# Kernel tuning notes

Measured on AMD Instinct MI355X. Metric: run time of the kernel, lower is better.

The kernel has to match this reference:

```python
import jax, jax.numpy as jnp
import numpy as np

B, H, W, C = 4, 64, 64, 256
CK = C // 8  # f/g projection dim = 32


def setup_inputs() -> dict:
    key = jax.random.key(0)
    ks = jax.random.split(key, 4)
    x = jax.random.normal(ks[0], (B, H, W, C), dtype=jnp.float32)
    Wf = jax.random.normal(ks[1], (C, CK), dtype=jnp.float32) * (1.0 / np.sqrt(C))
    Wg = jax.random.normal(ks[2], (C, CK), dtype=jnp.float32) * (1.0 / np.sqrt(C))
    Wh = jax.random.normal(ks[3], (C, C), dtype=jnp.float32) * (1.0 / np.sqrt(C))
    bf = jnp.zeros((CK,), jnp.float32)
    bg = jnp.zeros((CK,), jnp.float32)
    bh = jnp.zeros((C,), jnp.float32)
    return {"x": x, "Wf": Wf, "bf": bf, "Wg": Wg, "bg": bg, "Wh": Wh, "bh": bh}


def reference(x, Wf, bf, Wg, bg, Wh, bh):
    b, h, w, c = x.shape
    n = h * w
    xf = x.reshape(b, n, c)  # 1x1 conv == per-pixel matmul
    f = xf @ Wf + bf         # [b, n, c/8]  (keys)
    g = xf @ Wg + bg         # [b, n, c/8]  (queries)
    hh = xf @ Wh + bh        # [b, n, c]    (values)
    # s[i,j] = g_i . f_j  (tf.matmul(g, f, transpose_b=True))
    s = jnp.einsum('bik,bjk->bij', g, f)
    beta = jax.nn.softmax(s, axis=-1)
    o = jnp.einsum('bij,bjc->bic', beta, hh)
    return x + o.reshape(b, h, w, c)
```

## Files before the change

kernel.cpp:

```cpp
#include <hip/hip_runtime.h>
#include <math.h>

#define CDIM 256
#define CKD  32
#define NPIX 4096
#define BATCH 4
#define NMACRO (NPIX / 64)

typedef __attribute__((ext_vector_type(8)))  short bf16x8;
typedef __attribute__((ext_vector_type(16))) float f32x16;

#if __has_builtin(__builtin_amdgcn_exp2f)
#define EXP2(x) __builtin_amdgcn_exp2f(x)
#else
#define EXP2(x) exp2f(x)
#endif

__device__ inline ushort f2bf(float x) {
    unsigned u = __float_as_uint(x);
    u += 0x7fffu + ((u >> 16) & 1u);
    return (ushort)(u >> 16);
}
__device__ inline unsigned packbf(float a, float b) {
    return (unsigned)f2bf(a) | ((unsigned)f2bf(b) << 16);
}
__device__ inline unsigned cvtpk(float a, float b) {
    unsigned r;
    asm("v_cvt_pk_bf16_f32 %0, %1, %2" : "=v"(r) : "v"(a), "v"(b));
    return r;
}
__device__ inline void lane32swap(unsigned &a, unsigned &b) {
    asm("v_permlane32_swap_b32 %0, %1" : "+v"(a), "+v"(b));
}

#define LDS_ASYNC16(gptr, lptr) \
  __builtin_amdgcn_global_load_lds((const __attribute__((address_space(1))) void*)(gptr), \
                                   (__attribute__((address_space(3))) void*)(lptr), 16, 0, 0)

__global__ __launch_bounds__(256) void prep_kernel(
    const float* __restrict__ Wh, const float* __restrict__ Wf,
    const float* __restrict__ Wg, ushort* __restrict__ Wt)
{
    __shared__ float ls[64 * 65];
    const int tid = threadIdx.x;
    const int bid = blockIdx.x;

    if (bid < 16) {
        const int k0 = (bid & 3) * 64, c0 = (bid >> 2) * 64;
        #pragma unroll
        for (int i = 0; i < 16; ++i) {
            int r = i * 4 + (tid >> 6), c = tid & 63;
            ls[r * 65 + c] = Wh[(k0 + r) * 256 + c0 + c];
        }
        __syncthreads();
        #pragma unroll
        for (int i = 0; i < 16; ++i) {
            int cr = i * 4 + (tid >> 6), k = tid & 63;
            Wt[(c0 + cr) * 256 + k0 + k] = f2bf(ls[k * 65 + cr]);
        }
    } else {
        const float* W = (bid == 16) ? Wf : Wg;
        const int rbase = 256 + (bid - 16) * 32;
        #pragma unroll
        for (int kh2 = 0; kh2 < 2; ++kh2) {
            __syncthreads();
            #pragma unroll
            for (int i = 0; i < 16; ++i) {
                int flat = i * 256 + tid;
                int k = flat >> 5, c = flat & 31;
                ls[c * 129 + k] = W[(kh2 * 128 + k) * 32 + c];
            }
            __syncthreads();
            #pragma unroll
            for (int i = 0; i < 16; ++i) {
                int flat = i * 256 + tid;
                int c = flat >> 7, k = flat & 127;
                Wt[(rbase + c) * 256 + kh2 * 128 + k] = f2bf(ls[c * 129 + k]);
            }
        }
    }
}

__global__ __launch_bounds__(256) void proj_kernel(
    const float*  __restrict__ x,
    const ushort* __restrict__ Wt,
    const float*  __restrict__ bfp, const float* __restrict__ bgp,
    const float*  __restrict__ bhp,
    ushort* __restrict__ fo,
    ushort* __restrict__ go,
    ushort* __restrict__ glo,
    ushort* __restrict__ ht)
{
    __shared__ ushort wls[2][1280 * 8];
    __shared__ ushort xls[2][128 * 8];

    const int tid  = threadIdx.x;
    const int w    = tid >> 6;
    const int lane = tid & 63;
    const int hl   = lane >> 5;
    const int ln   = lane & 31;
    const int bid  = blockIdx.x;
    const long long px0 = (long long)bid * 32;
    const int b    = (int)(px0 >> 12);
    const int n0   = (int)(px0 & (NPIX - 1));
    const int kt   = n0 >> 6;
    const int koff = n0 & 63;

    const int sx_px = tid >> 3, sx_j = tid & 7;
    const int sx_o = sx_j >> 1, sx_h = sx_j & 1;
    const int sx_slot = sx_o * 32 + ((sx_px + 2 * sx_o) & 31);

    #pragma unroll
    for (int i = 0; i < 5; ++i) {
        int s = i * 256 + tid;
        int n = s >> 2, o = ((s & 3) - (n >> 1)) & 3;
        LDS_ASYNC16(Wt + n * 256 + o * 8, &wls[0][s * 8]);
    }
    {
        float4 v = *(const float4*)(x + (px0 + sx_px) * CDIM + sx_j * 4);
        uint2 p; p.x = packbf(v.x, v.y); p.y = packbf(v.z, v.w);
        *(uint2*)&xls[0][sx_slot * 8 + sx_h * 4] = p;
    }

    f32x16 acc0={0,0,0,0,0,0,0,0,0,0,0,0,0,0,0,0};
    f32x16 acc1={0,0,0,0,0,0,0,0,0,0,0,0,0,0,0,0};
    f32x16 accfg={0,0,0,0,0,0,0,0,0,0,0,0,0,0,0,0};

    for (int sl = 0; sl < 8; ++sl) {
        const int cur = sl & 1;
        __syncthreads();
        if (sl + 1 < 8) {
            const int nxt = cur ^ 1;
            #pragma unroll
            for (int i = 0; i < 5; ++i) {
                int s = i * 256 + tid;
                int n = s >> 2, o = ((s & 3) - (n >> 1)) & 3;
                LDS_ASYNC16(Wt + n * 256 + (sl + 1) * 32 + o * 8, &wls[nxt][s * 8]);
            }
            float4 v = *(const float4*)(x + (px0 + sx_px) * CDIM + (sl + 1) * 32 + sx_j * 4);
            uint2 p; p.x = packbf(v.x, v.y); p.y = packbf(v.z, v.w);
            *(uint2*)&xls[nxt][sx_slot * 8 + sx_h * 4] = p;
        }

        #pragma unroll
        for (int st = 0; st < 2; ++st) {
            const int o = st * 2 + hl;
            #define LDW(n) (*(const bf16x8*)&wls[cur][((n) * 4 + (((o) + ((n) >> 1)) & 3)) * 8])
            bf16x8 xb  = *(const bf16x8*)&xls[cur][(o * 32 + ((ln + 2 * o) & 31)) * 8];
            bf16x8 wa0 = LDW(w * 64 + ln);
            bf16x8 wa1 = LDW(w * 64 + 32 + ln);
            acc0 = __builtin_amdgcn_mfma_f32_32x32x16_bf16(wa0, xb, acc0, 0, 0, 0);
            acc1 = __builtin_amdgcn_mfma_f32_32x32x16_bf16(wa1, xb, acc1, 0, 0, 0);
            if (w < 2) {
                bf16x8 wfg = LDW(256 + w * 32 + ln);
                accfg = __builtin_amdgcn_mfma_f32_32x32x16_bf16(xb, wfg, accfg, 0, 0, 0);
            }
            #undef LDW
        }
    }

    ushort* htt = ht + ((long long)(b * 64 + kt) * CDIM) * 64 + koff;
    #pragma unroll
    for (int r = 0; r < 16; ++r) {
        const int rowD = (r & 3) + 8 * (r >> 2) + 4 * hl;
        int c0 = w * 64 + rowD, c1 = c0 + 32;
        htt[(long long)c0 * 64 + ln] = f2bf(acc0[r] + bhp[c0]);
        htt[(long long)c1 * 64 + ln] = f2bf(acc1[r] + bhp[c1]);
    }
    if (w < 2) {
        const float bb = (w ? bgp : bfp)[ln];
        const float scl = w ? 1.44269504088896f : 1.0f;
        #pragma unroll
        for (int r = 0; r < 16; ++r) {
            const int rowD = (r & 3) + 8 * (r >> 2) + 4 * hl;
            float v = (accfg[r] + bb) * scl;
            ushort hi = f2bf(v);
            long long idx = (px0 + rowD) * CKD + ln;
            if (w == 0) {
                fo[idx] = hi;
            } else {
                go[idx] = hi;
                float hif = __uint_as_float(((unsigned)hi) << 16);
                glo[idx] = f2bf(v - hif);
            }
        }
    }
}

__global__ __launch_bounds__(256, 3) void attn_kernel(
    const float*  __restrict__ x,
    const ushort* __restrict__ fk,
    const ushort* __restrict__ gq,
    const ushort* __restrict__ glo,
    const ushort* __restrict__ hv,
    float* __restrict__ out,
    float* __restrict__ Opart,
    float* __restrict__ Lpart,
    int nks)
{
    __shared__ ushort hh_lds[2][1024 * 8];
    __shared__ ushort f_lds[2][256 * 8];
    __shared__ float  l_red[2][64];

    const int tid  = threadIdx.x;
    const int w    = tid >> 6;
    const int lane = tid & 63;
    const int hl   = lane >> 5;
    const int ln   = lane & 31;

    const int bid = blockIdx.x;
    const int chs = bid & 1;
    const int b   = (bid >> 1) & 3;
    const int rest = bid >> 3;
    const int qt  = rest & 63;
    const int ks  = rest >> 6;
    const int q0  = qt * 64;
    const int kt0 = (ks * NMACRO) / nks;
    const int kt1 = ((ks + 1) * NMACRO) / nks;
    const int nmac = kt1 - kt0;

    const int qb = w & 1;
    const int kh = w >> 1;

    const long long bbase = (long long)b * NPIX;
    const ushort* fbase = fk + bbase * CKD;
    const ushort* htb   = hv + (long long)b * 64 * (CDIM * 64);

    const ushort* gp  = gq  + (bbase + q0 + qb * 32 + ln) * CKD;
    const ushort* glp = glo + (bbase + q0 + qb * 32 + ln) * CKD;
    const bf16x8 ga0 = *(const bf16x8*)(gp + hl * 8);
    const bf16x8 ga1 = *(const bf16x8*)(gp + 16 + hl * 8);
    const bf16x8 gl0 = *(const bf16x8*)(glp + hl * 8);
    const bf16x8 gl1 = *(const bf16x8*)(glp + 16 + hl * 8);

    {
        const long long tb = (long long)kt0 * (CDIM * 64);
        #pragma unroll
        for (int i = 0; i < 4; ++i) {
            int s = i * 256 + tid;
            int c = s >> 3, j = ((s & 7) - c) & 7;
            LDS_ASYNC16(htb + tb + (long long)(chs * 128 + c) * 64 + j * 8, &hh_lds[0][s * 8]);
        }
        LDS_ASYNC16(fbase + (long long)(kt0 * 64 + (tid & 63)) * CKD + (tid >> 6) * 8,
                    &f_lds[0][tid * 8]);
    }

    const f32x16 Zv = {0,0,0,0,0,0,0,0,0,0,0,0,0,0,0,0};
    f32x16 acc0={0,0,0,0,0,0,0,0,0,0,0,0,0,0,0,0};
    f32x16 acc1={0,0,0,0,0,0,0,0,0,0,0,0,0,0,0,0};
    f32x16 acc2={0,0,0,0,0,0,0,0,0,0,0,0,0,0,0,0};
    f32x16 acc3={0,0,0,0,0,0,0,0,0,0,0,0,0,0,0,0};
    float lsA = 0.f, lsB = 0.f;

    #pragma unroll 2
    for (int m = 0; m < nmac; ++m) {
        const int kt = kt0 + m;
        const int cur = m & 1;
        __syncthreads();

        if (m + 1 < nmac) {
            const int nxt = cur ^ 1;
            const long long tb = (long long)(kt + 1) * (CDIM * 64);
            #pragma unroll
            for (int i = 0; i < 4; ++i) {
                int s = i * 256 + tid;
                int c = s >> 3, j = ((s & 7) - c) & 7;
                LDS_ASYNC16(htb + tb + (long long)(chs * 128 + c) * 64 + j * 8,
                            &hh_lds[nxt][s * 8]);
            }
            LDS_ASYNC16(fbase + (long long)((kt + 1) * 64 + (tid & 63)) * CKD + (tid >> 6) * 8,
                        &f_lds[nxt][tid * 8]);
        }

        f32x16 S;
        {
            bf16x8 fb0 = *(const bf16x8*)&f_lds[cur][((hl)     * 64 + kh * 32 + ln) * 8];
            bf16x8 fb1 = *(const bf16x8*)&f_lds[cur][((2 + hl) * 64 + kh * 32 + ln) * 8];
            __builtin_amdgcn_s_setprio(1);
            S = __builtin_amdgcn_mfma_f32_32x32x16_bf16(fb0, ga0, Zv, 0, 0, 0);
            S = __builtin_amdgcn_mfma_f32_32x32x16_bf16(fb0, gl0, S, 0, 0, 0);
            S = __builtin_amdgcn_mfma_f32_32x32x16_bf16(fb1, ga1, S, 0, 0, 0);
            S = __builtin_amdgcn_mfma_f32_32x32x16_bf16(fb1, gl1, S, 0, 0, 0);
            __builtin_amdgcn_s_setprio(0);
        }

        float p[16];
        #pragma unroll
        for (int r = 0; r < 16; ++r) {
            p[r] = EXP2(S[r]);
            if (r & 1) lsB += p[r]; else lsA += p[r];
        }
        unsigned U[8];
        #pragma unroll
        for (int m2 = 0; m2 < 8; ++m2) U[m2] = cvtpk(p[2*m2], p[2*m2+1]);

        #pragma unroll
        for (int ck = 0; ck < 2; ++ck) {
            unsigned a0 = U[4*ck + 0], a1 = U[4*ck + 1];
            unsigned a2 = U[4*ck + 2], a3 = U[4*ck + 3];
            lane32swap(a0, a2);
            lane32swap(a1, a3);
            union { unsigned i[4]; bf16x8 v; } pf;
            pf.i[0] = a0; pf.i[1] = a1; pf.i[2] = a2; pf.i[3] = a3;
            bf16x8 pa = pf.v;
            const int oct = kh * 4 + ck * 2 + hl;
            const int c0 = ln, c1 = 32 + ln, c2 = 64 + ln, c3 = 96 + ln;
            bf16x8 hb0 = *(const bf16x8*)&hh_lds[cur][(c0 * 8 + ((oct + c0) & 7)) * 8];
            bf16x8 hb1 = *(const bf16x8*)&hh_lds[cur][(c1 * 8 + ((oct + c1) & 7)) * 8];
            bf16x8 hb2 = *(const bf16x8*)&hh_lds[cur][(c2 * 8 + ((oct + c2) & 7)) * 8];
            bf16x8 hb3 = *(const bf16x8*)&hh_lds[cur][(c3 * 8 + ((oct + c3) & 7)) * 8];
            __builtin_amdgcn_s_setprio(1);
            acc0 = __builtin_amdgcn_mfma_f32_32x32x16_bf16(pa, hb0, acc0, 0, 0, 0);
            acc1 = __builtin_amdgcn_mfma_f32_32x32x16_bf16(pa, hb1, acc1, 0, 0, 0);
            acc2 = __builtin_amdgcn_mfma_f32_32x32x16_bf16(pa, hb2, acc2, 0, 0, 0);
            acc3 = __builtin_amdgcn_mfma_f32_32x32x16_bf16(pa, hb3, acc3, 0, 0, 0);
            __builtin_amdgcn_s_setprio(0);
        }
    }

    float lsum = lsA + lsB;
    lsum += __shfl_xor(lsum, 32);
    __syncthreads();
    if (hl == 0) l_red[kh][qb * 32 + ln] = lsum;
    float* O_s = (float*)hh_lds;
    if (kh == 0) {
        #pragma unroll
        for (int r = 0; r < 16; ++r) {
            int rowD = (r & 3) + 8 * (r >> 2) + 4 * hl;
            O_s[((qb * 4 + 2) * 32 + rowD) * 32 + ln] = acc2[r];
            O_s[((qb * 4 + 3) * 32 + rowD) * 32 + ln] = acc3[r];
        }
    } else {
        #pragma unroll
        for (int r = 0; r < 16; ++r) {
            int rowD = (r & 3) + 8 * (r >> 2) + 4 * hl;
            O_s[((qb * 4 + 0) * 32 + rowD) * 32 + ln] = acc0[r];
            O_s[((qb * 4 + 1) * 32 + rowD) * 32 + ln] = acc1[r];
        }
    }
    __syncthreads();

    if (Opart) {
        const long long pb = ((long long)(ks * BATCH + b) * NPIX + q0);
        if (w == 0 && chs == 0)
            Lpart[pb + lane] = l_red[0][lane] + l_red[1][lane];
        if (kh == 0) {
            #pragma unroll
            for (int r = 0; r < 16; ++r) {
                int rowD = (r & 3) + 8 * (r >> 2) + 4 * hl;
                int ql = qb * 32 + rowD;
                long long rg = (pb + ql) * CDIM + chs * 128 + ln;
                Opart[rg]      = acc0[r] + O_s[((qb * 4 + 0) * 32 + rowD) * 32 + ln];
                Opart[rg + 32] = acc1[r] + O_s[((qb * 4 + 1) * 32 + rowD) * 32 + ln];
            }
        } else {
            #pragma unroll
            for (int r = 0; r < 16; ++r) {
                int rowD = (r & 3) + 8 * (r >> 2) + 4 * hl;
                int ql = qb * 32 + rowD;
                long long rg = (pb + ql) * CDIM + chs * 128 + 64 + ln;
                Opart[rg]      = acc2[r] + O_s[((qb * 4 + 2) * 32 + rowD) * 32 + ln];
                Opart[rg + 32] = acc3[r] + O_s[((qb * 4 + 3) * 32 + rowD) * 32 + ln];
            }
        }
    } else {
        if (kh == 0) {
            #pragma unroll
            for (int r = 0; r < 16; ++r) {
                int rowD = (r & 3) + 8 * (r >> 2) + 4 * hl;
                int ql = qb * 32 + rowD;
                float linv = 1.f / (l_red[0][ql] + l_red[1][ql]);
                long long rg = (bbase + q0 + ql) * CDIM + chs * 128 + ln;
                float o0 = acc0[r] + O_s[((qb * 4 + 0) * 32 + rowD) * 32 + ln];
                float o1 = acc1[r] + O_s[((qb * 4 + 1) * 32 + rowD) * 32 + ln];
                out[rg]      = x[rg]      + o0 * linv;
                out[rg + 32] = x[rg + 32] + o1 * linv;
            }
        } else {
            #pragma unroll
            for (int r = 0; r < 16; ++r) {
                int rowD = (r & 3) + 8 * (r >> 2) + 4 * hl;
                int ql = qb * 32 + rowD;
                float linv = 1.f / (l_red[0][ql] + l_red[1][ql]);
                long long rg = (bbase + q0 + ql) * CDIM + chs * 128 + 64 + ln;
                float o2 = acc2[r] + O_s[((qb * 4 + 2) * 32 + rowD) * 32 + ln];
                float o3 = acc3[r] + O_s[((qb * 4 + 3) * 32 + rowD) * 32 + ln];
                out[rg]      = x[rg]      + o2 * linv;
                out[rg + 32] = x[rg + 32] + o3 * linv;
            }
        }
    }
}

__global__ __launch_bounds__(256) void combine_kernel(
    const float* __restrict__ x, const float* __restrict__ Op,
    const float* __restrict__ Lp, float* __restrict__ out, int nks)
{
    const int tid = threadIdx.x, w = tid >> 6, lane = tid & 63;
    const int row = blockIdx.x * 4 + w;
    const int b = row >> 12, q = row & (NPIX - 1);

    float l = 0.f;
    for (int ks = 0; ks < nks; ++ks)
        l += Lp[(ks * BATCH + b) * NPIX + q];
    const float linv = 1.f / l;

    float4 a = {0.f, 0.f, 0.f, 0.f};
    for (int ks = 0; ks < nks; ++ks) {
        const float4 v = *(const float4*)&Op[
            (((long long)(ks * BATCH + b) * NPIX + q)) * CDIM + lane * 4];
        a.x += v.x; a.y += v.y; a.z += v.z; a.w += v.w;
    }
    const long long g = ((long long)b * NPIX + q) * CDIM + lane * 4;
    const float4 xv = *(const float4*)&x[g];
    float4 o;
    o.x = xv.x + a.x * linv;
    o.y = xv.y + a.y * linv;
    o.z = xv.z + a.z * linv;
    o.w = xv.w + a.w * linv;
    *(float4*)&out[g] = o;
}

extern "C" void kernel_launch(void* const* d_in, const int* in_sizes, int n_in,
                              void* d_out, int out_size, void* d_ws, size_t ws_size,
                              hipStream_t stream) {
    const float* x  = (const float*)d_in[0];
    const float* Wf = (const float*)d_in[1];
    const float* bf = (const float*)d_in[2];
    const float* Wg = (const float*)d_in[3];
    const float* bg = (const float*)d_in[4];
    const float* Wh = (const float*)d_in[5];
    const float* bh = (const float*)d_in[6];
    float* out = (float*)d_out;

    ushort* fbf = (ushort*)d_ws;
    ushort* gbf = fbf + BATCH * NPIX * CKD;
    ushort* glo = gbf + BATCH * NPIX * CKD;
    ushort* ht  = glo + BATCH * NPIX * CKD;
    ushort* Wt  = ht + BATCH * NPIX * CDIM;
    char*   pb  = (char*)(Wt + 320 * 256);

    const int NKS = 3;
    const size_t base_used = (size_t)(pb - (char*)d_ws);
    const size_t oelems = (size_t)NKS * BATCH * NPIX * CDIM;
    const size_t lelems = (size_t)NKS * BATCH * NPIX;
    float* Opart = nullptr;
    float* Lpart = nullptr;
    int nks = 1;
    if (ws_size >= base_used + (oelems + lelems) * sizeof(float)) {
        nks = NKS;
        Opart = (float*)pb;
        Lpart = Opart + oelems;
    }

    prep_kernel<<<dim3(18), 256, 0, stream>>>(Wh, Wf, Wg, Wt);
    proj_kernel<<<dim3(512), 256, 0, stream>>>(x, Wt, bf, bg, bh, fbf, gbf, glo, ht);
    attn_kernel<<<dim3(512 * nks), 256, 0, stream>>>(x, fbf, gbf, glo, ht, out,
                                                     Opart, Lpart, nks);
    if (nks > 1)
        combine_kernel<<<dim3(BATCH * NPIX / 4), 256, 0, stream>>>(x, Opart, Lpart, out, nks);
}
```

Before: 168.1 us.

## Give each wave its own 32 query rows and loop over key halves

Each wave now owns 32 query rows and iterates over both 32-key halves of a macro tile, so a block covers 128 queries and the grid is halved. Every K/V tile loaded into LDS therefore serves twice as many queries, and the LDS cross-wave reduction of partial outputs and its extra barrier are removed. The hi/lo query score MFMAs now run as two independent chains that are summed before the exp, which shortens the dependency chain. In exchange there are fewer blocks in flight and each wave does more serial work per tile.

```diff
diff --git a/kernel.cpp b/kernel.cpp
--- a/kernel.cpp
+++ b/kernel.cpp
@@ -200,7 +200,7 @@
 {
     __shared__ ushort hh_lds[2][1024 * 8];
     __shared__ ushort f_lds[2][256 * 8];
-    __shared__ float  l_red[2][64];
+    __shared__ float  l_red[128];
 
     const int tid  = threadIdx.x;
     const int w    = tid >> 6;
@@ -211,23 +211,19 @@
     const int bid = blockIdx.x;
     const int chs = bid & 1;
     const int b   = (bid >> 1) & 3;
-    const int rest = bid >> 3;
-    const int qt  = rest & 63;
-    const int ks  = rest >> 6;
-    const int q0  = qt * 64;
+    const int qt  = (bid >> 3) & 31;
+    const int ks  = bid >> 8;
+    const int q0  = qt * 128;
     const int kt0 = (ks * NMACRO) / nks;
     const int kt1 = ((ks + 1) * NMACRO) / nks;
     const int nmac = kt1 - kt0;
 
-    const int qb = w & 1;
-    const int kh = w >> 1;
-
     const long long bbase = (long long)b * NPIX;
     const ushort* fbase = fk + bbase * CKD;
     const ushort* htb   = hv + (long long)b * 64 * (CDIM * 64);
 
-    const ushort* gp  = gq  + (bbase + q0 + qb * 32 + ln) * CKD;
-    const ushort* glp = glo + (bbase + q0 + qb * 32 + ln) * CKD;
+    const ushort* gp  = gq  + (bbase + q0 + w * 32 + ln) * CKD;
+    const ushort* glp = glo + (bbase + q0 + w * 32 + ln) * CKD;
     const bf16x8 ga0 = *(const bf16x8*)(gp + hl * 8);
     const bf16x8 ga1 = *(const bf16x8*)(gp + 16 + hl * 8);
     const bf16x8 gl0 = *(const bf16x8*)(glp + hl * 8);
@@ -272,122 +268,84 @@
                         &f_lds[nxt][tid * 8]);
         }
 
-        f32x16 S;
-        {
-            bf16x8 fb0 = *(const bf16x8*)&f_lds[cur][((hl)     * 64 + kh * 32 + ln) * 8];
-            bf16x8 fb1 = *(const bf16x8*)&f_lds[cur][((2 + hl) * 64 + kh * 32 + ln) * 8];
-            __builtin_amdgcn_s_setprio(1);
-            S = __builtin_amdgcn_mfma_f32_32x32x16_bf16(fb0, ga0, Zv, 0, 0, 0);
-            S = __builtin_amdgcn_mfma_f32_32x32x16_bf16(fb0, gl0, S, 0, 0, 0);
-            S = __builtin_amdgcn_mfma_f32_32x32x16_bf16(fb1, ga1, S, 0, 0, 0);
-            S = __builtin_amdgcn_mfma_f32_32x32x16_bf16(fb1, gl1, S, 0, 0, 0);
-            __builtin_amdgcn_s_setprio(0);
-        }
-
-        float p[16];
-        #pragma unroll
-        for (int r = 0; r < 16; ++r) {
-            p[r] = EXP2(S[r]);
-            if (r & 1) lsB += p[r]; else lsA += p[r];
-        }
-        unsigned U[8];
-        #pragma unroll
-        for (int m2 = 0; m2 < 8; ++m2) U[m2] = cvtpk(p[2*m2], p[2*m2+1]);
-
-        #pragma unroll
-        for (int ck = 0; ck < 2; ++ck) {
-            unsigned a0 = U[4*ck + 0], a1 = U[4*ck + 1];
-            unsigned a2 = U[4*ck + 2], a3 = U[4*ck + 3];
-            lane32swap(a0, a2);
-            lane32swap(a1, a3);
-            union { unsigned i[4]; bf16x8 v; } pf;
-            pf.i[0] = a0; pf.i[1] = a1; pf.i[2] = a2; pf.i[3] = a3;
-            bf16x8 pa = pf.v;
-            const int oct = kh * 4 + ck * 2 + hl;
-            const int c0 = ln, c1 = 32 + ln, c2 = 64 + ln, c3 = 96 + ln;
-            bf16x8 hb0 = *(const bf16x8*)&hh_lds[cur][(c0 * 8 + ((oct + c0) & 7)) * 8];
-            bf16x8 hb1 = *(const bf16x8*)&hh_lds[cur][(c1 * 8 + ((oct + c1) & 7)) * 8];
-            bf16x8 hb2 = *(const bf16x8*)&hh_lds[cur][(c2 * 8 + ((oct + c2) & 7)) * 8];
-            bf16x8 hb3 = *(const bf16x8*)&hh_lds[cur][(c3 * 8 + ((oct + c3) & 7)) * 8];
-            __builtin_amdgcn_s_setprio(1);
-            acc0 = __builtin_amdgcn_mfma_f32_32x32x16_bf16(pa, hb0, acc0, 0, 0, 0);
-            acc1 = __builtin_amdgcn_mfma_f32_32x32x16_bf16(pa, hb1, acc1, 0, 0, 0);
-            acc2 = __builtin_amdgcn_mfma_f32_32x32x16_bf16(pa, hb2, acc2, 0, 0, 0);
-            acc3 = __builtin_amdgcn_mfma_f32_32x32x16_bf16(pa, hb3, acc3, 0, 0, 0);
-            __builtin_amdgcn_s_setprio(0);
+        #pragma unroll
+        for (int kh = 0; kh < 2; ++kh) {
+            f32x16 S, T;
+            {
+                bf16x8 fb0 = *(const bf16x8*)&f_lds[cur][((hl)     * 64 + kh * 32 + ln) * 8];
+                bf16x8 fb1 = *(const bf16x8*)&f_lds[cur][((2 + hl) * 64 + kh * 32 + ln) * 8];
+                __builtin_amdgcn_s_setprio(1);
+                S = __builtin_amdgcn_mfma_f32_32x32x16_bf16(fb0, ga0, Zv, 0, 0, 0);
+                T = __builtin_amdgcn_mfma_f32_32x32x16_bf16(fb0, gl0, Zv, 0, 0, 0);
+                S = __builtin_amdgcn_mfma_f32_32x32x16_bf16(fb1, ga1, S, 0, 0, 0);
+                T = __builtin_amdgcn_mfma_f32_32x32x16_bf16(fb1, gl1, T, 0, 0, 0);
+                __builtin_amdgcn_s_setprio(0);
+            }
+
+            float p[16];
+            #pragma unroll
+            for (int r = 0; r < 16; ++r) {
+                p[r] = EXP2(S[r] + T[r]);
+                if (r & 1) lsB += p[r]; else lsA += p[r];
+            }
+            unsigned U[8];
+            #pragma unroll
+            for (int m2 = 0; m2 < 8; ++m2) U[m2] = cvtpk(p[2*m2], p[2*m2+1]);
+
+            #pragma unroll
+            for (int ck = 0; ck < 2; ++ck) {
+                unsigned a0 = U[4*ck + 0], a1 = U[4*ck + 1];
+                unsigned a2 = U[4*ck + 2], a3 = U[4*ck + 3];
+                lane32swap(a0, a2);
+                lane32swap(a1, a3);
+                union { unsigned i[4]; bf16x8 v; } pf;
+                pf.i[0] = a0; pf.i[1] = a1; pf.i[2] = a2; pf.i[3] = a3;
+                bf16x8 pa = pf.v;
+                const int oct = kh * 4 + ck * 2 + hl;
+                const int c0 = ln, c1 = 32 + ln, c2 = 64 + ln, c3 = 96 + ln;
+                bf16x8 hb0 = *(const bf16x8*)&hh_lds[cur][(c0 * 8 + ((oct + c0) & 7)) * 8];
+                bf16x8 hb1 = *(const bf16x8*)&hh_lds[cur][(c1 * 8 + ((oct + c1) & 7)) * 8];
+                bf16x8 hb2 = *(const bf16x8*)&hh_lds[cur][(c2 * 8 + ((oct + c2) & 7)) * 8];
+                bf16x8 hb3 = *(const bf16x8*)&hh_lds[cur][(c3 * 8 + ((oct + c3) & 7)) * 8];
+                __builtin_amdgcn_s_setprio(1);
+                acc0 = __builtin_amdgcn_mfma_f32_32x32x16_bf16(pa, hb0, acc0, 0, 0, 0);
+                acc1 = __builtin_amdgcn_mfma_f32_32x32x16_bf16(pa, hb1, acc1, 0, 0, 0);
+                acc2 = __builtin_amdgcn_mfma_f32_32x32x16_bf16(pa, hb2, acc2, 0, 0, 0);
+                acc3 = __builtin_amdgcn_mfma_f32_32x32x16_bf16(pa, hb3, acc3, 0, 0, 0);
+                __builtin_amdgcn_s_setprio(0);
+            }
         }
     }
 
     float lsum = lsA + lsB;
     lsum += __shfl_xor(lsum, 32);
+    if (hl == 0) l_red[w * 32 + ln] = lsum;
     __syncthreads();
-    if (hl == 0) l_red[kh][qb * 32 + ln] = lsum;
-    float* O_s = (float*)hh_lds;
-    if (kh == 0) {
+
+    if (Opart) {
+        const long long pb = ((long long)(ks * BATCH + b) * NPIX + q0);
+        if (chs == 0 && hl == 0) Lpart[pb + w * 32 + ln] = lsum;
         #pragma unroll
         for (int r = 0; r < 16; ++r) {
             int rowD = (r & 3) + 8 * (r >> 2) + 4 * hl;
-            O_s[((qb * 4 + 2) * 32 + rowD) * 32 + ln] = acc2[r];
-            O_s[((qb * 4 + 3) * 32 + rowD) * 32 + ln] = acc3[r];
+            int ql = w * 32 + rowD;
+            long long rg = (pb + ql) * CDIM + chs * 128 + ln;
+            Opart[rg]      = acc0[r];
+            Opart[rg + 32] = acc1[r];
+            Opart[rg + 64] = acc2[r];
+            Opart[rg + 96] = acc3[r];
         }
     } else {
         #pragma unroll
         for (int r = 0; r < 16; ++r) {
             int rowD = (r & 3) + 8 * (r >> 2) + 4 * hl;
-            O_s[((qb * 4 + 0) * 32 + rowD) * 32 + ln] = acc0[r];
-            O_s[((qb * 4 + 1) * 32 + rowD) * 32 + ln] = acc1[r];
-        }
-    }
-    __syncthreads();
-
-    if (Opart) {
-        const long long pb = ((long long)(ks * BATCH + b) * NPIX + q0);
-        if (w == 0 && chs == 0)
-            Lpart[pb + lane] = l_red[0][lane] + l_red[1][lane];
-        if (kh == 0) {
-            #pragma unroll
-            for (int r = 0; r < 16; ++r) {
-                int rowD = (r & 3) + 8 * (r >> 2) + 4 * hl;
-                int ql = qb * 32 + rowD;
-                long long rg = (pb + ql) * CDIM + chs * 128 + ln;
-                Opart[rg]      = acc0[r] + O_s[((qb * 4 + 0) * 32 + rowD) * 32 + ln];
-                Opart[rg + 32] = acc1[r] + O_s[((qb * 4 + 1) * 32 + rowD) * 32 + ln];
-            }
-        } else {
-            #pragma unroll
-            for (int r = 0; r < 16; ++r) {
-                int rowD = (r & 3) + 8 * (r >> 2) + 4 * hl;
-                int ql = qb * 32 + rowD;
-                long long rg = (pb + ql) * CDIM + chs * 128 + 64 + ln;
-                Opart[rg]      = acc2[r] + O_s[((qb * 4 + 2) * 32 + rowD) * 32 + ln];
-                Opart[rg + 32] = acc3[r] + O_s[((qb * 4 + 3) * 32 + rowD) * 32 + ln];
-            }
-        }
-    } else {
-        if (kh == 0) {
-            #pragma unroll
-            for (int r = 0; r < 16; ++r) {
-                int rowD = (r & 3) + 8 * (r >> 2) + 4 * hl;
-                int ql = qb * 32 + rowD;
-                float linv = 1.f / (l_red[0][ql] + l_red[1][ql]);
-                long long rg = (bbase + q0 + ql) * CDIM + chs * 128 + ln;
-                float o0 = acc0[r] + O_s[((qb * 4 + 0) * 32 + rowD) * 32 + ln];
-                float o1 = acc1[r] + O_s[((qb * 4 + 1) * 32 + rowD) * 32 + ln];
-                out[rg]      = x[rg]      + o0 * linv;
-                out[rg + 32] = x[rg + 32] + o1 * linv;
-            }
-        } else {
-            #pragma unroll
-            for (int r = 0; r < 16; ++r) {
-                int rowD = (r & 3) + 8 * (r >> 2) + 4 * hl;
-                int ql = qb * 32 + rowD;
-                float linv = 1.f / (l_red[0][ql] + l_red[1][ql]);
-                long long rg = (bbase + q0 + ql) * CDIM + chs * 128 + 64 + ln;
-                float o2 = acc2[r] + O_s[((qb * 4 + 2) * 32 + rowD) * 32 + ln];
-                float o3 = acc3[r] + O_s[((qb * 4 + 3) * 32 + rowD) * 32 + ln];
-                out[rg]      = x[rg]      + o2 * linv;
-                out[rg + 32] = x[rg + 32] + o3 * linv;
-            }
+            int ql = w * 32 + rowD;
+            float linv = 1.f / l_red[ql];
+            long long rg = (bbase + q0 + ql) * CDIM + chs * 128 + ln;
+            out[rg]      = x[rg]      + acc0[r] * linv;
+            out[rg + 32] = x[rg + 32] + acc1[r] * linv;
+            out[rg + 64] = x[rg + 64] + acc2[r] * linv;
+            out[rg + 96] = x[rg + 96] + acc3[r] * linv;
         }
     }
 }
@@ -455,7 +413,7 @@
 
     prep_kernel<<<dim3(18), 256, 0, stream>>>(Wh, Wf, Wg, Wt);
     proj_kernel<<<dim3(512), 256, 0, stream>>>(x, Wt, bf, bg, bh, fbf, gbf, glo, ht);
-    attn_kernel<<<dim3(512 * nks), 256, 0, stream>>>(x, fbf, gbf, glo, ht, out,
+    attn_kernel<<<dim3(256 * nks), 256, 0, stream>>>(x, fbf, gbf, glo, ht, out,
                                                      Opart, Lpart, nks);
     if (nks > 1)
         combine_kernel<<<dim3(BATCH * NPIX / 4), 256, 0, stream>>>(x, Opart, Lpart, out, nks);
```

After: 159.7 us. -5.0%, faster.
